# Optimization experiments

Measured on AMD Instinct MI355X. Metric: run time of the kernel, lower is better.

The kernel has to match this reference:

```python
import jax, jax.numpy as jnp
import numpy as np
from jax.scipy.linalg import expm

T, N, M_IN, DT = 8192, 1024, 512, 0.01


def setup_inputs() -> dict:
    key = jax.random.key(0)
    kA, kB, ky, ku = jax.random.split(key, 4)
    ts = jnp.arange(T, dtype=jnp.float32) * DT
    # Mildly stable dynamics so the trajectory stays bounded over T steps.
    A = 0.1 * jax.random.normal(kA, (N, N), jnp.float32) / np.sqrt(N) - 0.5 * jnp.eye(N, dtype=jnp.float32)
    B = jax.random.normal(kB, (N, M_IN), jnp.float32) / np.sqrt(M_IN)
    y0 = jax.random.normal(ky, (N,), jnp.float32)
    u = jax.random.normal(ku, (T, M_IN), jnp.float32)
    return {"ts": ts, "y0": y0, "u": u, "A": A, "B": B}


def reference(ts, y0, u, A, B):
    # Exact solution of dy/dt = A y + B u(t) with u piecewise-linear on ts
    # (what diffrax Tsit5+PID approximates to rtol=1e-3). Uses Van Loan's
    # augmented matrix exponential: z = [y; u; v] with u' = v, v' = 0.
    n = A.shape[0]
    m = B.shape[1]
    h = ts[1] - ts[0]  # uniform grid
    Z_nm = jnp.zeros((n, m), A.dtype)
    Mblk = jnp.block([
        [A, B, Z_nm],
        [jnp.zeros((m, n + m), A.dtype), jnp.eye(m, dtype=A.dtype)],
        [jnp.zeros((m, n + 2 * m), A.dtype)],
    ])
    E = expm(Mblk * h)
    Eyy = E[:n, :n]            # state transition e^{Ah}
    Eyu = E[:n, n:n + m]       # response to constant input u_k
    Eyv = E[:n, n + m:]        # response to input slope v_k
    v = (u[1:] - u[:-1]) / h                     # [T-1, m] slopes
    c = u[:-1] @ Eyu.T + v @ Eyv.T               # [T-1, n] affine terms

    def step(y, ck):
        y_next = Eyy @ y + ck
        return y_next, y_next

    _, ys = jax.lax.scan(step, y0, c)
    return jnp.concatenate([y0[None, :], ys], axis=0)  # [T, n]
```

## Files before the change

### kernel.cpp

```cpp
#include <hip/hip_runtime.h>

#define GT 8192
#define GN 1024
#define GM 512
#define CCH 1024
#define SCH 8

typedef __attribute__((ext_vector_type(8))) short bf16x8;
typedef __attribute__((ext_vector_type(4))) float f32x4;

__device__ __forceinline__ unsigned short f2bf(float x) {
    unsigned int u = __float_as_uint(x);
    u += 0x7FFF + ((u >> 16) & 1);
    return (unsigned short)(u >> 16);
}
__device__ __forceinline__ float bf2f(unsigned short b) {
    return __uint_as_float(((unsigned int)b) << 16);
}
__device__ __forceinline__ void split2(float x, unsigned short& h0, unsigned short& h1) {
    h0 = f2bf(x);
    h1 = f2bf(x - bf2f(h0));
}
__device__ __forceinline__ void split3(float x, unsigned short& s0,
                                       unsigned short& s1, unsigned short& s2) {
    s0 = f2bf(x); float r = x - bf2f(s0);
    s1 = f2bf(r); r -= bf2f(s1);
    s2 = f2bf(r);
}
__device__ __forceinline__ long swz(long e, int sh) {
    return e ^ (((e >> (sh + 1)) & 3) << 3);
}
__device__ __forceinline__ void gl16(const unsigned short* g, unsigned short* l) {
    __builtin_amdgcn_global_load_lds(
        (const __attribute__((address_space(1))) unsigned int*)g,
        (__attribute__((address_space(3))) unsigned int*)l, 16, 0, 0);
}

template <int BM, int WN, int KS>
__global__ __launch_bounds__(512) void gemm_pp(
    const unsigned short* __restrict__ Ap, long apsz, int alda, int aldsh,
    int ashift, int ashiftN,
    const unsigned short* __restrict__ Bp, long bpsz,
    const float* __restrict__ Cf, long cfb, long cfld,
    const unsigned short* __restrict__ Cp, long cpsz, int cmask,
    int bzero, int bsplit, float beta, float betaB,
    float* __restrict__ Of, long ofb, long ofld,
    unsigned short* __restrict__ Pout, long ppsz, int pstep8, int pmode,
    int segN, int zoff,
    int M, float alpha, float alphaB, int asplit, int add_id,
    const unsigned short* __restrict__ Ap2, long apsz2,
    const unsigned short* __restrict__ Bp2,
    unsigned short* __restrict__ Pout2, long ppsz2, int p2off, int seg2,
    unsigned short* __restrict__ PoutT, int tposeN)
{
    constexpr int NQ = 2 * WN;
    constexpr int MTM = BM / 32;
    constexpr int MTN = BM / (WN * 16);
    constexpr int CPW = KS * BM / 32;
    __shared__ __align__(16) unsigned short At[2][KS][2][BM][32];
    __shared__ __align__(16) unsigned short Bt[2][KS][2][BM][32];

    const int tid = threadIdx.x;
    const int lane = tid & 63;
    const int w = tid >> 6;
    const int ksub = w / NQ;
    const int quad = w % NQ;
    const int wr = (quad / WN) * (BM / 2);
    const int wc = (quad % WN) * (BM / WN);
    const int l16 = lane & 15, koff = lane >> 4;
    const int row0 = blockIdx.x * BM;
    const int col0 = blockIdx.y * BM;
    const int lr4 = lane >> 2;
    const int lg = lane & 3;
    const bool s2 = (Ap2 != nullptr) && (row0 >= seg2);
    const bool lead = (KS == 1) || (ksub == 0);

    f32x4 acc[MTM][MTN] = {};

    auto stage = [&](int bsel, int k0) {
        #pragma unroll
        for (int ci = 0; ci < CPW; ++ci) {
            const int c = w * CPW + ci;
            const int op = c / (KS * BM / 8);
            const int rem = c % (KS * BM / 8);
            const int limb = rem / (KS * BM / 16);
            const int rem2 = rem % (KS * BM / 16);
            const int kk = rem2 / (BM / 16);
            const int rb = (rem2 % (BM / 16)) * 16;
            const int lr = rb + lr4;
            const int q = lg ^ ((lr >> 1) & 3);
            long e; int sh; const unsigned short* base;
            if (op == 0) {
                if (!s2) {
                    int ar = row0 + lr;
                    if (ar < ashiftN) { ar -= ashift; if (ar < 0) ar = 0; }
                    e = (long)ar * alda + k0 + kk * 32 + (q << 3); sh = aldsh;
                    base = Ap + (limb ? apsz : 0);
                } else {
                    e = (long)(row0 - seg2 + lr) * 1024 + k0 + kk * 32 + (q << 3); sh = 10;
                    base = Ap2 + (limb ? apsz2 : 0);
                }
            } else {
                e = (long)(col0 + lr) * 1024 + k0 + kk * 32 + (q << 3); sh = 10;
                base = (s2 ? Bp2 : Bp) + (limb ? bpsz : 0);
            }
            long f = swz(e, sh);
            unsigned short* l = (op == 0 ? &At[bsel][kk][limb][rb][0]
                                         : &Bt[bsel][kk][limb][rb][0]);
            gl16(base + f, l);
        }
    };

    stage(0, 0);
    __syncthreads();
    int cur = 0;
    for (int k0 = 0; k0 < 1024; k0 += KS * 32) {
        if (k0 + KS * 32 < 1024) stage(cur ^ 1, k0 + KS * 32);

        const int kk = ksub;
        bf16x8 a0[MTM], a1[MTM], b0[MTN], b1[MTN];
        #pragma unroll
        for (int mi = 0; mi < MTM; ++mi) {
            int lr = wr + mi * 16 + l16;
            int off = (koff ^ ((lr >> 1) & 3)) << 3;
            a0[mi] = *(const bf16x8*)&At[cur][kk][0][lr][off];
            a1[mi] = *(const bf16x8*)&At[cur][kk][1][lr][off];
        }
        #pragma unroll
        for (int ni = 0; ni < MTN; ++ni) {
            int lr = wc + ni * 16 + l16;
            int off = (koff ^ ((lr >> 1) & 3)) << 3;
            b0[ni] = *(const bf16x8*)&Bt[cur][kk][0][lr][off];
            b1[ni] = *(const bf16x8*)&Bt[cur][kk][1][lr][off];
        }
        #pragma unroll
        for (int mi = 0; mi < MTM; ++mi)
            #pragma unroll
            for (int ni = 0; ni < MTN; ++ni) {
                f32x4 cc = acc[mi][ni];
                cc = __builtin_amdgcn_mfma_f32_16x16x32_bf16(a0[mi], b0[ni], cc, 0, 0, 0);
                cc = __builtin_amdgcn_mfma_f32_16x16x32_bf16(a0[mi], b1[ni], cc, 0, 0, 0);
                cc = __builtin_amdgcn_mfma_f32_16x16x32_bf16(a1[mi], b0[ni], cc, 0, 0, 0);
                acc[mi][ni] = cc;
            }
        __syncthreads();
        cur ^= 1;
    }

    if (KS == 2) {
        float* red = (float*)&At[0][0][0][0][0];
        if (ksub == 1) {
            #pragma unroll
            for (int mi = 0; mi < MTM; ++mi)
                #pragma unroll
                for (int ni = 0; ni < MTN; ++ni)
                    *(f32x4*)&red[(((quad * MTM + mi) * MTN + ni) * 64 + lane) * 4] =
                        acc[mi][ni];
        }
        __syncthreads();
        if (ksub == 0) {
            #pragma unroll
            for (int mi = 0; mi < MTM; ++mi)
                #pragma unroll
                for (int ni = 0; ni < MTN; ++ni) {
                    f32x4 o = *(const f32x4*)
                        &red[(((quad * MTM + mi) * MTN + ni) * 64 + lane) * 4];
                    acc[mi][ni][0] += o[0]; acc[mi][ni][1] += o[1];
                    acc[mi][ni][2] += o[2]; acc[mi][ni][3] += o[3];
                }
        }
    }

    const bool tp = (PoutT != nullptr) && (row0 >= tposeN);
    float* T = (float*)&Bt[0][0][0][0][0];

    if (s2) {
        if (lead) {
            #pragma unroll
            for (int mi = 0; mi < MTM; ++mi)
                #pragma unroll
                for (int r = 0; r < 4; ++r) {
                    const int gr = row0 + wr + mi * 16 + koff * 4 + r;
                    if (gr >= M) continue;
                    const int prow = gr - seg2 + p2off;
                    #pragma unroll
                    for (int ni = 0; ni < MTN; ++ni) {
                        const int gc = col0 + wc + ni * 16 + l16;
                        float pv = acc[mi][ni][r];
                        long f = swz((long)prow * 1024 + gc, 10);
                        unsigned short h0 = f2bf(pv);
                        Pout2[f] = h0;
                        Pout2[ppsz2 + f] = f2bf(pv - bf2f(h0));
                        if (tp) T[(wr + mi * 16 + koff * 4 + r) * 65 + gc - col0] = pv;
                    }
                }
        }
    } else {
        if (lead) {
            #pragma unroll
            for (int mi = 0; mi < MTM; ++mi) {
                #pragma unroll
                for (int r = 0; r < 4; ++r) {
                    const int gr = row0 + wr + mi * 16 + koff * 4 + r;
                    if (gr >= M) continue;
                    const int trow = (gr < segN) ? gr + zoff : gr;
                    if (gr < segN && trow >= segN) continue;
                    const float aa = (trow < asplit) ? alpha : alphaB;
                    const float bb = (trow < bzero) ? 0.f
                                    : ((trow < bsplit) ? beta : betaB);
                    #pragma unroll
                    for (int ni = 0; ni < MTN; ++ni) {
                        const int gc = col0 + wc + ni * 16 + l16;
                        float vp = aa * acc[mi][ni][r];
                        float v = vp;
                        if (bb != 0.f) {
                            int crow = trow & cmask;
                            if (Cf) v += bb * Cf[cfb + (long)crow * cfld + gc];
                            else if (Cp) {
                                long f = swz((long)crow * 1024 + gc, 10);
                                v += bb * (bf2f(Cp[f]) + bf2f(Cp[cpsz + f]));
                            }
                        }
                        if (add_id && gr == gc) v += 1.f;
                        if (Of) Of[ofb + (long)trow * ofld + gc] = v;
                        if (Pout && (!pstep8 || (trow & 7) == 0)) {
                            int prow = pstep8 ? (trow >> 3) : trow;
                            long f = swz((long)prow * 1024 + gc, 10);
                            float pv = (pmode == 2) ? vp : v;
                            unsigned short h0 = f2bf(pv);
                            Pout[f] = h0;
                            Pout[ppsz + f] = f2bf(pv - bf2f(h0));
                        }
                        if (tp) T[(wr + mi * 16 + koff * 4 + r) * 65 + gc - col0] = v;
                    }
                }
            }
        }
    }

    if (BM == 64 && tp) {
        __syncthreads();
        if (tid < 256) {
            const int i = tid >> 2;
            const int jb = (tid & 3) * 16;
            const int prow = col0 + i;
            #pragma unroll
            for (int e2 = 0; e2 < 16; ++e2) {
                int j = jb + e2;
                float v = T[j * 65 + i];
                long f = swz((long)prow * 1024 + (row0 - tposeN + j), 10);
                unsigned short h0 = f2bf(v);
                PoutT[f] = h0;
                PoutT[(long)(1 << 20) + f] = f2bf(v - bf2f(h0));
            }
        }
    }
}

__global__ void split_pl_k(const float* __restrict__ X, unsigned short* __restrict__ P,
                           long psz, int ldsh, float s, long cnt)
{
    long i = (long)blockIdx.x * 256 + threadIdx.x;
    if (i >= cnt) return;
    float v = s * X[i];
    long f = swz(i, ldsh);
    unsigned short h0 = f2bf(v);
    P[f] = h0;
    P[psz + f] = f2bf(v - bf2f(h0));
}

__global__ void trsp_k(const float* __restrict__ in, int R, float s, int add_id,
                       unsigned short* __restrict__ P, long psz, int roff)
{
    __shared__ float t[32][33];
    const int tx = threadIdx.x & 31, ty4 = threadIdx.x >> 5;
    const int r0 = blockIdx.x * 32, c0 = blockIdx.y * 32;
    #pragma unroll
    for (int i = 0; i < 4; ++i)
        t[ty4 * 4 + i][tx] = in[(long)(c0 + ty4 * 4 + i) * R + r0 + tx];
    __syncthreads();
    #pragma unroll
    for (int i = 0; i < 4; ++i) {
        int r = r0 + ty4 * 4 + i, c = c0 + tx;
        float v = s * t[tx][ty4 * 4 + i];
        if (add_id && r == c) v += 1.f;
        long f = swz((long)(r + roff) * 1024 + c, 10);
        unsigned short h0 = f2bf(v);
        P[f] = h0;
        P[psz + f] = f2bf(v - bf2f(h0));
    }
}

__global__ void tspp_k(const unsigned short* __restrict__ IN, long ipsz, long irow0,
                       unsigned short* __restrict__ OUT, long opsz)
{
    __shared__ float t[32][33];
    const int tx = threadIdx.x & 31, ty4 = threadIdx.x >> 5;
    const int r0 = blockIdx.x * 32, c0 = blockIdx.y * 32;
    #pragma unroll
    for (int i = 0; i < 4; ++i) {
        long f = swz((irow0 + r0 + ty4 * 4 + i) * 1024 + c0 + tx, 10);
        t[ty4 * 4 + i][tx] = bf2f(IN[f]) + bf2f(IN[ipsz + f]);
    }
    __syncthreads();
    #pragma unroll
    for (int i = 0; i < 4; ++i) {
        int orow = c0 + ty4 * 4 + i;
        long f = swz((long)orow * 1024 + r0 + tx, 10);
        float v = t[tx][ty4 * 4 + i];
        unsigned short h0 = f2bf(v);
        OUT[f] = h0;
        OUT[opsz + f] = f2bf(v - bf2f(h0));
    }
}

__global__ void gtspp_k(const unsigned short* __restrict__ PV, long vpsz,
                        unsigned short* __restrict__ PG, long gpsz, float h)
{
    __shared__ float t[32][33];
    const int tx = threadIdx.x & 31, ty4 = threadIdx.x >> 5;
    const int k0 = blockIdx.x * 32, n0 = blockIdx.y * 32, z = blockIdx.z;
    #pragma unroll
    for (int i = 0; i < 4; ++i) {
        int k = k0 + ty4 * 4 + i, n = n0 + tx;
        long f2 = swz((long)(512 + k) * 1024 + n, 10);
        float v2 = bf2f(PV[f2]) + bf2f(PV[vpsz + f2]);
        float v;
        if (z == 0) {
            long f1 = swz((long)k * 1024 + n, 10);
            v = h * (bf2f(PV[f1]) + bf2f(PV[vpsz + f1]) - v2);
        } else v = h * v2;
        t[ty4 * 4 + i][tx] = v;
    }
    __syncthreads();
    #pragma unroll
    for (int i = 0; i < 4; ++i) {
        int n = n0 + ty4 * 4 + i, kk = z * 512 + k0 + tx;
        long f = swz((long)n * 1024 + kk, 10);
        float v = t[tx][ty4 * 4 + i];
        unsigned short h0 = f2bf(v);
        PG[f] = h0;
        PG[gpsz + f] = f2bf(v - bf2f(h0));
    }
}

__global__ void copy_rows_k(float* __restrict__ dst, long db, long ds,
                            const float* __restrict__ src, long sb, long ss, int ncols)
{
    int r = blockIdx.y;
    int c = blockIdx.x * 256 + threadIdx.x;
    if (c < ncols) dst[db + (long)r * ds + c] = src[sb + (long)r * ss + c];
}

__global__ void add_rows_k(float* __restrict__ dst, long db, long ds,
                           const float* __restrict__ src, int ncols)
{
    int r = blockIdx.y;
    int c = blockIdx.x * 256 + threadIdx.x;
    if (c < ncols) dst[db + (long)r * ds + c] += src[(long)r * ncols + c];
}

__global__ void scale_add_id_k(float* __restrict__ dst, const float* __restrict__ src,
                               float s, int n)
{
    int r = blockIdx.y;
    int c = blockIdx.x * 256 + threadIdx.x;
    if (c < n) dst[(long)r * n + c] = s * src[(long)r * n + c] + ((r == c) ? 1.f : 0.f);
}

__global__ void scale_copy_k(float* __restrict__ dst, const float* __restrict__ src,
                             float s, long cnt)
{
    long i = (long)blockIdx.x * 256 + threadIdx.x;
    if (i < cnt) dst[i] = s * src[i];
}

__global__ void g1g2_k(float* __restrict__ g1, float* __restrict__ g2,
                       const float* __restrict__ v1, const float* __restrict__ v2,
                       float h, long cnt)
{
    long i = (long)blockIdx.x * 256 + threadIdx.x;
    if (i < cnt) {
        float a = v1[i], b = v2[i];
        g1[i] = h * (a - b);
        g2[i] = h * b;
    }
}

template <int BM, int BN, bool TRANSB>
__global__ __launch_bounds__(256) void gemm_mfma(
    const float* __restrict__ A, long ab, long lda,
    const float* __restrict__ B,
    const float* __restrict__ Cin, long cb, long ldc, float beta,
    float* __restrict__ Out, long ob, long ldo,
    int M, int Nn, int K, float alpha, int add_id)
{
    constexpr int LDT = 40;
    __shared__ unsigned short At[3][BM][LDT];
    __shared__ unsigned short Bt[3][BN][LDT];
    const int tid = threadIdx.x;
    const int lane = tid & 63;
    const int wid = tid >> 6;
    const int row0 = blockIdx.x * BM;
    const int col0 = blockIdx.y * BN;
    constexpr int MR = BM / 32;
    constexpr int NR = BN / 32;
    const int wrow = (wid >> 1) * (BM / 2);
    const int wcol = (wid & 1) * (BN / 2);
    const int l16 = lane & 15;
    const int koff = lane >> 4;
    f32x4 acc[MR][NR] = {};

    for (int k0 = 0; k0 < K; k0 += 32) {
        #pragma unroll
        for (int i = 0; i < BM / 32; ++i) {
            int r = i * 32 + (tid >> 3);
            int kl = (tid & 7) * 4;
            int gr = row0 + r;
            float4 v = make_float4(0.f, 0.f, 0.f, 0.f);
            if (gr < M) v = *(const float4*)&A[ab + (long)gr * lda + (k0 + kl)];
            unsigned short h0[4], h1[4], h2[4];
            split3(v.x, h0[0], h1[0], h2[0]);
            split3(v.y, h0[1], h1[1], h2[1]);
            split3(v.z, h0[2], h1[2], h2[2]);
            split3(v.w, h0[3], h1[3], h2[3]);
            *(ushort4*)&At[0][r][kl] = make_ushort4(h0[0], h0[1], h0[2], h0[3]);
            *(ushort4*)&At[1][r][kl] = make_ushort4(h1[0], h1[1], h1[2], h1[3]);
            *(ushort4*)&At[2][r][kl] = make_ushort4(h2[0], h2[1], h2[2], h2[3]);
        }
        if (TRANSB) {
            #pragma unroll
            for (int i = 0; i < BN / 32; ++i) {
                int r = i * 32 + (tid >> 3);
                int kl = (tid & 7) * 4;
                float4 v = *(const float4*)&B[(long)(col0 + r) * K + (k0 + kl)];
                unsigned short h0[4], h1[4], h2[4];
                split3(v.x, h0[0], h1[0], h2[0]);
                split3(v.y, h0[1], h1[1], h2[1]);
                split3(v.z, h0[2], h1[2], h2[2]);
                split3(v.w, h0[3], h1[3], h2[3]);
                *(ushort4*)&Bt[0][r][kl] = make_ushort4(h0[0], h0[1], h0[2], h0[3]);
                *(ushort4*)&Bt[1][r][kl] = make_ushort4(h1[0], h1[1], h1[2], h1[3]);
                *(ushort4*)&Bt[2][r][kl] = make_ushort4(h2[0], h2[1], h2[2], h2[3]);
            }
        } else {
            constexpr int TPK = BN / 4;
            #pragma unroll
            for (int i = 0; i < BN / 32; ++i) {
                int kl = i * (256 / TPK) + tid / TPK;
                int nl = (tid % TPK) * 4;
                float4 v = *(const float4*)&B[(long)(k0 + kl) * Nn + (col0 + nl)];
                unsigned short s0, s1, s2;
                split3(v.x, s0, s1, s2);
                Bt[0][nl + 0][kl] = s0; Bt[1][nl + 0][kl] = s1; Bt[2][nl + 0][kl] = s2;
                split3(v.y, s0, s1, s2);
                Bt[0][nl + 1][kl] = s0; Bt[1][nl + 1][kl] = s1; Bt[2][nl + 1][kl] = s2;
                split3(v.z, s0, s1, s2);
                Bt[0][nl + 2][kl] = s0; Bt[1][nl + 2][kl] = s1; Bt[2][nl + 2][kl] = s2;
                split3(v.w, s0, s1, s2);
                Bt[0][nl + 3][kl] = s0; Bt[1][nl + 3][kl] = s1; Bt[2][nl + 3][kl] = s2;
            }
        }
        __syncthreads();
        bf16x8 bf[NR][3];
        #pragma unroll
        for (int nr = 0; nr < NR; ++nr) {
            int brow = wcol + nr * 16 + l16;
            #pragma unroll
            for (int s = 0; s < 3; ++s)
                bf[nr][s] = *(const bf16x8*)&Bt[s][brow][koff * 8];
        }
        #pragma unroll
        for (int mr = 0; mr < MR; ++mr) {
            int arow = wrow + mr * 16 + l16;
            bf16x8 a0 = *(const bf16x8*)&At[0][arow][koff * 8];
            bf16x8 a1 = *(const bf16x8*)&At[1][arow][koff * 8];
            bf16x8 a2 = *(const bf16x8*)&At[2][arow][koff * 8];
            #pragma unroll
            for (int nr = 0; nr < NR; ++nr) {
                f32x4 c = acc[mr][nr];
                c = __builtin_amdgcn_mfma_f32_16x16x32_bf16(a0, bf[nr][0], c, 0, 0, 0);
                c = __builtin_amdgcn_mfma_f32_16x16x32_bf16(a0, bf[nr][1], c, 0, 0, 0);
                c = __builtin_amdgcn_mfma_f32_16x16x32_bf16(a1, bf[nr][0], c, 0, 0, 0);
                c = __builtin_amdgcn_mfma_f32_16x16x32_bf16(a0, bf[nr][2], c, 0, 0, 0);
                c = __builtin_amdgcn_mfma_f32_16x16x32_bf16(a1, bf[nr][1], c, 0, 0, 0);
                c = __builtin_amdgcn_mfma_f32_16x16x32_bf16(a2, bf[nr][0], c, 0, 0, 0);
                acc[mr][nr] = c;
            }
        }
        __syncthreads();
    }
    #pragma unroll
    for (int mr = 0; mr < MR; ++mr) {
        #pragma unroll
        for (int r = 0; r < 4; ++r) {
            int gr = row0 + wrow + mr * 16 + koff * 4 + r;
            if (gr >= M) continue;
            #pragma unroll
            for (int nr = 0; nr < NR; ++nr) {
                int gc = col0 + wcol + nr * 16 + l16;
                float v = alpha * acc[mr][nr][r];
                if (Cin) v += beta * Cin[cb + (long)gr * ldc + gc];
                if (add_id && gr == gc) v += 1.f;
                Out[ob + (long)gr * ldo + gc] = v;
            }
        }
    }
}

static void fallback_launch(void* const* d_in, void* d_out, void* d_ws,
                            hipStream_t stream)
{
    const float* y0 = (const float*)d_in[1];
    const float* u  = (const float*)d_in[2];
    const float* Am = (const float*)d_in[3];
    const float* Bm = (const float*)d_in[4];
    float* Yout = (float*)d_out;
    float* w = (float*)d_ws;
    const float h = 0.01f;
    const int N = GN;

    float* Eyy = w;
    float* T1  = Eyy + (long)N * N;
    float* T2  = T1  + (long)N * N;
    float* V1  = T2  + (long)N * N;
    float* Vt  = V1  + (long)N * GM;
    float* V2  = Vt  + (long)N * GM;
    float* G1  = V2  + (long)N * GM;
    float* G2  = G1  + (long)N * GM;
    float* Z   = G2  + (long)N * GM;
    float* Zt  = Z   + (long)CCH * N;
    dim3 blk(256);

    auto gemm = [&](bool transb, const float* A, long ab, long lda,
                    const float* B, const float* Cin, long cb, long ldc, float beta,
                    float* Out, long ob, long ldo,
                    int M, int Nn, int K, float alpha, int add_id) {
        if (M > 1536 && (Nn % 128) == 0) {
            dim3 grid((M + 127) / 128, Nn / 128);
            if (transb)
                gemm_mfma<128, 128, true><<<grid, blk, 0, stream>>>(A, ab, lda, B, Cin, cb, ldc, beta, Out, ob, ldo, M, Nn, K, alpha, add_id);
            else
                gemm_mfma<128, 128, false><<<grid, blk, 0, stream>>>(A, ab, lda, B, Cin, cb, ldc, beta, Out, ob, ldo, M, Nn, K, alpha, add_id);
        } else {
            dim3 grid((M + 63) / 64, Nn / 64);
            if (transb)
                gemm_mfma<64, 64, true><<<grid, blk, 0, stream>>>(A, ab, lda, B, Cin, cb, ldc, beta, Out, ob, ldo, M, Nn, K, alpha, add_id);
            else
                gemm_mfma<64, 64, false><<<grid, blk, 0, stream>>>(A, ab, lda, B, Cin, cb, ldc, beta, Out, ob, ldo, M, Nn, K, alpha, add_id);
        }
    };

    scale_add_id_k<<<dim3(4, N), blk, 0, stream>>>(T1, Am, h / 5.f, N);
    {
        float* pc = T1; float* pn = T2;
        for (int k = 4; k >= 1; --k) {
            float* out = (k == 1) ? Eyy : pn;
            gemm(false, Am, 0, N, pc, nullptr, 0, 0, 0.f, out, 0, N, N, N, N, h / (float)k, 1);
            pn = pc; pc = out;
        }
    }
    const long NM = (long)N * GM;
    scale_copy_k<<<dim3((unsigned)((NM + 255) / 256)), blk, 0, stream>>>(V1, Bm, 1.f / 120.f, NM);
    {
        const float f1[4] = {1.f / 24.f, 1.f / 6.f, 0.5f, 1.f};
        float* pc = V1; float* pn = Vt;
        for (int j = 3; j >= 0; --j) {
            gemm(false, Am, 0, N, pc, Bm, 0, GM, f1[3 - j], pn, 0, GM, N, GM, N, h, 0);
            float* t = pc; pc = pn; pn = t;
        }
    }
    scale_copy_k<<<dim3((unsigned)((NM + 255) / 256)), blk, 0, stream>>>(V2, Bm, 1.f / 720.f, NM);
    {
        const float f2[4] = {1.f / 120.f, 1.f / 24.f, 1.f / 6.f, 0.5f};
        float* pc = V2; float* pn = Vt;
        for (int j = 3; j >= 0; --j) {
            gemm(false, Am, 0, N, pc, Bm, 0, GM, f2[3 - j], pn, 0, GM, N, GM, N, h, 0);
            float* t = pc; pc = pn; pn = t;
        }
    }
    g1g2_k<<<dim3((unsigned)((NM + 255) / 256)), blk, 0, stream>>>(G1, G2, V1, V2, h, NM);
    gemm(true, u, 0, GM, G1, nullptr, 0, 0, 0.f, Yout, (long)N, N, GT - 1, N, GM, 1.f, 0);
    gemm(true, u, GM, GM, G2, Yout, (long)N, N, 1.f, Yout, (long)N, N, GT - 1, N, GM, 1.f, 0);
    copy_rows_k<<<dim3(4, 1), blk, 0, stream>>>(Yout, 0, 0, y0, 0, 0, N);
    for (int s = 2; s <= SCH; ++s) {
        int Mr = (GT - 1 - s) / SCH + 1;
        gemm(true, Yout, (long)(s - 1) * N, (long)SCH * N, Eyy,
             Yout, (long)s * N, (long)SCH * N, 1.f,
             Yout, (long)s * N, (long)SCH * N, Mr, N, N, 1.f, 0);
    }
    copy_rows_k<<<dim3(4, 1), blk, 0, stream>>>(Z, 0, 0, y0, 0, 0, N);
    copy_rows_k<<<dim3(4, CCH - 1), blk, 0, stream>>>(Z, (long)N, (long)N,
                                                      Yout, (long)SCH * N, (long)SCH * N, N);
    gemm(false, Eyy, 0, N, Eyy, nullptr, 0, 0, 0.f, T1, 0, N, N, N, N, 1.f, 0);
    gemm(false, T1, 0, N, T1, nullptr, 0, 0, 0.f, T2, 0, N, N, N, N, 1.f, 0);
    gemm(false, T2, 0, N, T2, nullptr, 0, 0, 0.f, T1, 0, N, N, N, N, 1.f, 0);
    {
        float* Mc = T1; float* Mo = T2;
        float* Zc = Z;  float* Zn = Zt;
        for (int p = 0; p < 10; ++p) {
            int o = 1 << p;
            gemm(true, Zc, 0, N, Mc, Zc, (long)o * N, N, 1.f,
                 Zn, (long)o * N, N, CCH - o, N, N, 1.f, 0);
            copy_rows_k<<<dim3(4, o), blk, 0, stream>>>(Zn, 0, N, Zc, 0, N, N);
            if (p < 9) {
                gemm(false, Mc, 0, N, Mc, nullptr, 0, 0, 0.f, Mo, 0, N, N, N, N, 1.f, 0);
                float* t = Mc; Mc = Mo; Mo = t;
            }
            float* t = Zc; Zc = Zn; Zn = t;
        }
        copy_rows_k<<<dim3(4, CCH), blk, 0, stream>>>(Yout, 0, (long)SCH * N, Zc, 0, N, N);
        float* Q = Zc; float* Qt = Zn;
        for (int s = 1; s <= SCH - 1; ++s) {
            gemm(true, Q, 0, N, Eyy, nullptr, 0, 0, 0.f, Qt, 0, N, CCH, N, N, 1.f, 0);
            int Mr = (GT - 1 - s) / SCH + 1;
            add_rows_k<<<dim3(4, Mr), blk, 0, stream>>>(Yout, (long)s * N, (long)SCH * N, Qt, N);
            float* t = Q; Q = Qt; Qt = t;
        }
    }
}

extern "C" void kernel_launch(void* const* d_in, const int* in_sizes, int n_in,
                              void* d_out, int out_size, void* d_ws, size_t ws_size,
                              hipStream_t stream)
{
    (void)in_sizes; (void)n_in; (void)out_size;
    const size_t NEED = 46ull * 1024 * 1024;
    if (ws_size < NEED) { fallback_launch(d_in, d_out, d_ws, stream); return; }

    const float* y0 = (const float*)d_in[1];
    const float* u  = (const float*)d_in[2];
    const float* Am = (const float*)d_in[3];
    const float* Bm = (const float*)d_in[4];
    float* Yout = (float*)d_out;
    char* w = (char*)d_ws;
    const float h = 0.01f;
    const size_t MB = 1024 * 1024;
    const long P1M = 1 << 20;
    const long P2M = 1 << 21;
    const long PUS = 1 << 22;
    const long PBS = 1 << 19;
    const int  BIG = 1 << 30;

    unsigned short* PU   = (unsigned short*)(w);
    unsigned short* PZW1 = (unsigned short*)(w);
    unsigned short* PZW2 = (unsigned short*)(w + 8 * MB);
    unsigned short* CH1  = (unsigned short*)(w + 16 * MB);
    unsigned short* SQb  = (unsigned short*)(w + 16 * MB);
    unsigned short* PWb  = (unsigned short*)(w + 20 * MB);
    unsigned short* CH2  = (unsigned short*)(w + 24 * MB);
    unsigned short* PY1  = (unsigned short*)(w + 24 * MB);
    unsigned short* PY2  = (unsigned short*)(w + 28 * MB);
    unsigned short* PE   = (unsigned short*)(w + 32 * MB);
    unsigned short* PG   = (unsigned short*)(w + 36 * MB);
    unsigned short* SQa  = PG;
    unsigned short* PA   = (unsigned short*)(w + 40 * MB);
    unsigned short* PWa  = PA;
    unsigned short* PBT  = (unsigned short*)(w + 44 * MB);

    dim3 blk(256), blk5(512);

    auto G64 = [&](const unsigned short* Ap, long apsz, int alda, int aldsh,
                   int ashift, int ashiftN,
                   const unsigned short* Bp,
                   const float* Cf, long cfb, long cfld,
                   const unsigned short* Cp, long cpsz, int cmask,
                   int bzero, int bsplit, float beta, float betaB,
                   float* Of, long ofb, long ofld,
                   unsigned short* Pout, long ppsz, int pstep8, int pmode,
                   int segN, int zoff, int M, float alpha, float alphaB,
                   int asplit, int add_id,
                   const unsigned short* Ap2, long apsz2, const unsigned short* Bp2,
                   unsigned short* Pout2, long ppsz2, int p2off, int seg2,
                   unsigned short* PoutT, int tposeN) {
        dim3 grid((M + 63) / 64, 16);
        gemm_pp<64, 2, 2><<<grid, blk5, 0, stream>>>(
            Ap, apsz, alda, aldsh, ashift, ashiftN, Bp, P1M,
            Cf, cfb, cfld, Cp, cpsz, cmask, bzero, bsplit, beta, betaB,
            Of, ofb, ofld, Pout, ppsz, pstep8, pmode, segN, zoff,
            M, alpha, alphaB, asplit, add_id,
            Ap2, apsz2, Bp2, Pout2, ppsz2, p2off, seg2, PoutT, tposeN);
    };

    split_pl_k<<<dim3(4096), blk, 0, stream>>>(Am, PA, P1M, 10, 1.f, (long)1 << 20);

    trsp_k<<<dim3(32, 32), blk, 0, stream>>>(Am, 1024, h / 5.f, 1, CH1, P2M, 0);
    trsp_k<<<dim3(16, 32), blk, 0, stream>>>(Bm, 512, 1.f / 120.f, 0, CH1, P2M, 1024);
    trsp_k<<<dim3(16, 32), blk, 0, stream>>>(Bm, 512, 1.f / 720.f, 0, CH1, P2M, 1536);
    trsp_k<<<dim3(16, 32), blk, 0, stream>>>(Bm, 512, 1.f, 0, PBT, PBS, 0);

    {
        const float alE[4] = {h / 4.f, h / 3.f, h / 2.f, h};
        const float f1[4] = {1.f / 24.f, 1.f / 6.f, 0.5f, 1.f};
        const float f2[4] = {1.f / 120.f, 1.f / 24.f, 1.f / 6.f, 0.5f};
        unsigned short* cc = CH1; unsigned short* cn = CH2;
        for (int j = 0; j < 4; ++j) {
            G64(cc, P2M, 1024, 10, 0, 0, PA,
                nullptr, 0, 0, PBT, PBS, 511,
                1024, 1536, f1[j], f2[j],
                nullptr, 0, 0, cn, P2M, 0, 1,
                BIG, 0, 2048, alE[j], h, 1024, 1,
                nullptr, 0, nullptr, nullptr, 0, 0, BIG, nullptr, BIG);
            unsigned short* t = cc; cc = cn; cn = t;
        }
    }
    tspp_k<<<dim3(32, 32), blk, 0, stream>>>(CH1, P2M, 0, PE, P1M);
    gtspp_k<<<dim3(16, 32, 2), blk, 0, stream>>>(CH1 + (1 << 20), P2M, PG, P1M, h);

    split_pl_k<<<dim3(16384), blk, 0, stream>>>(u, PU, PUS, 9, 1.f, PUS);

    gemm_pp<128, 4, 1><<<dim3(64, 8), blk5, 0, stream>>>(
        PU, PUS, 512, 9, 0, 0, PG, P1M,
        nullptr, 0, 0, nullptr, 0, -1, 0, BIG, 0.f, 0.f,
        Yout, 1024, 1024, PY1, P1M, 1, 1,
        BIG, 0, GT - 1, 1.f, 1.f, BIG, 0,
        nullptr, 0, nullptr, nullptr, 0, 0, BIG, nullptr, BIG);
    copy_rows_k<<<dim3(4, 1), blk, 0, stream>>>(Yout, 0, 0, y0, 0, 0, 1024);

    G64(PY1, P1M, 1024, 10, 0, 0, PE,
        Yout, 2 * 1024, 8192, nullptr, 0, -1, 0, BIG, 1.f, 0.f,
        Yout, 2 * 1024, 8192, PY2, P1M, 0, 1,
        BIG, 0, 2048, 1.f, 1.f, BIG, 0,
        CH1, P2M, PE, SQa, P1M, 0, 1024, PWa, 1024);
    G64(PY2, P1M, 1024, 10, 0, 0, PE,
        Yout, 3 * 1024, 8192, nullptr, 0, -1, 0, BIG, 1.f, 0.f,
        Yout, 3 * 1024, 8192, PY1, P1M, 0, 1,
        BIG, 0, 2048, 1.f, 1.f, BIG, 0,
        SQa, P1M, PWa, SQb, P1M, 0, 1024, PWb, 1024);
    G64(PY1, P1M, 1024, 10, 0, 0, PE,
        Yout, 4 * 1024, 8192, nullptr, 0, -1, 0, BIG, 1.f, 0.f,
        Yout, 4 * 1024, 8192, PY2, P1M, 0, 1,
        BIG, 0, 2048, 1.f, 1.f, BIG, 0,
        SQb, P1M, PWb, PZW1, P2M, 1024, 1024, PWa, 1024);
    {
        unsigned short* pc = PY2; unsigned short* pn = PY1;
        for (int s = 5; s <= 7; ++s) {
            G64(pc, P1M, 1024, 10, 0, 0, PE,
                Yout, (long)s * 1024, 8192, nullptr, 0, -1, 0, BIG, 1.f, 0.f,
                Yout, (long)s * 1024, 8192, pn, P1M, 0, 1,
                BIG, 0, 1024, 1.f, 1.f, BIG, 0,
                nullptr, 0, nullptr, nullptr, 0, 0, BIG, nullptr, BIG);
            unsigned short* t = pc; pc = pn; pn = t;
        }
        G64(pc, P1M, 1024, 10, 0, 0, PE,
            Yout, 0, 8192, nullptr, 0, -1, 0, BIG, 1.f, 0.f,
            Yout, 0, 8192, PZW1, P2M, 0, 1,
            BIG, 1, 1023, 1.f, 1.f, BIG, 0,
            nullptr, 0, nullptr, nullptr, 0, 0, BIG, nullptr, BIG);
    }
    split_pl_k<<<dim3(4), blk, 0, stream>>>(y0, PZW1, P2M, 10, 1.f, 1024);

    {
        unsigned short* PZc = PZW1; unsigned short* PZn = PZW2;
        for (int p = 0; p < 10; ++p) {
            int o = 1 << p;
            unsigned short* PWcur = (p & 1) ? PWb : PWa;
            unsigned short* PWnxt = (p & 1) ? PWa : PWb;
            if (p < 9) {
                G64(PZc, P2M, 1024, 10, o, 1024, PWcur,
                    nullptr, 0, 0, PZc, P2M, 0x7fffffff,
                    0, 1024, 1.f, 0.f,
                    nullptr, 0, 0, PZn, P2M, 0, 1,
                    1024, 0, 2048, 0.f, 1.f, o, 0,
                    nullptr, 0, nullptr, nullptr, 0, 0, BIG, PWnxt, 1024);
            } else {
                G64(PZc, P2M, 1024, 10, o, 1024, PWcur,
                    nullptr, 0, 0, PZc, P2M, 0x7fffffff,
                    0, 1024, 1.f, 0.f,
                    Yout, 0, 8192, PZn, P2M, 0, 1,
                    1024, 0, 1024, 0.f, 1.f, o, 0,
                    nullptr, 0, nullptr, nullptr, 0, 0, BIG, nullptr, BIG);
            }
            unsigned short* t = PZc; PZc = PZn; PZn = t;
        }
    }
    copy_rows_k<<<dim3(4, 1), blk, 0, stream>>>(Yout, 0, 0, y0, 0, 0, 1024);

    {
        const unsigned short* pc = PZW1; long apsz = P2M;
        unsigned short* pn = PY1;
        for (int s = 1; s <= 7; ++s) {
            G64(pc, apsz, 1024, 10, 0, 0, PE,
                Yout, (long)s * 1024, 8192, nullptr, 0, -1, 0, BIG, 1.f, 0.f,
                Yout, (long)s * 1024, 8192,
                (s < 7) ? pn : nullptr, P1M, 0, 2,
                BIG, 0, 1024, 1.f, 1.f, BIG, 0,
                nullptr, 0, nullptr, nullptr, 0, 0, BIG, nullptr, BIG);
            pc = pn; apsz = P1M;
            pn = (pn == PY1) ? PY2 : PY1;
        }
    }
}
```

Before: 808.5 us.

## Batch final propagation steps using precomputed powers of the transition matrix

Adds segment-indexed B-matrix strides, row masks and output strides to the GEMM kernel, so one launch can apply different matrices to different 1024-row segments. The prologue now also computes extra powers of Eyy (PW2, PW3, PW4, via PWR=PE). The final seven serial propagation GEMMs become two wider batched launches: one multiplies by E^1..E^4 in parallel, the other applies E^4 to those results. This trades a serial launch chain for more parallel work per launch, with extra power-matrix computation, more workspace aliasing and some risk to accuracy.

```diff
diff --git a/kernel.cpp b/kernel.cpp
--- a/kernel.cpp
+++ b/kernel.cpp
@@ -39,14 +39,14 @@
 template <int BM, int WN, int KS>
 __global__ __launch_bounds__(512) void gemm_pp(
     const unsigned short* __restrict__ Ap, long apsz, int alda, int aldsh,
-    int ashift, int ashiftN,
-    const unsigned short* __restrict__ Bp, long bpsz,
+    int amask, int ashift, int ashiftN,
+    const unsigned short* __restrict__ Bp, long bpsz, long bstride,
     const float* __restrict__ Cf, long cfb, long cfld,
     const unsigned short* __restrict__ Cp, long cpsz, int cmask,
     int bzero, int bsplit, float beta, float betaB,
-    float* __restrict__ Of, long ofb, long ofld,
-    unsigned short* __restrict__ Pout, long ppsz, int pstep8, int pmode,
-    int segN, int zoff,
+    float* __restrict__ Of, long ofb, long ofld, long ofstep,
+    unsigned short* __restrict__ Pout, long ppsz, int pstep8, int pmode, int prowstep,
+    int segN, int zoff, int trmask,
     int M, float alpha, float alphaB, int asplit, int add_id,
     const unsigned short* __restrict__ Ap2, long apsz2,
     const unsigned short* __restrict__ Bp2,
@@ -74,6 +74,7 @@
     const int lg = lane & 3;
     const bool s2 = (Ap2 != nullptr) && (row0 >= seg2);
     const bool lead = (KS == 1) || (ksub == 0);
+    const int segk = row0 >> 10;
 
     f32x4 acc[MTM][MTN] = {};
 
@@ -92,7 +93,7 @@
             long e; int sh; const unsigned short* base;
             if (op == 0) {
                 if (!s2) {
-                    int ar = row0 + lr;
+                    int ar = (row0 + lr) & amask;
                     if (ar < ashiftN) { ar -= ashift; if (ar < 0) ar = 0; }
                     e = (long)ar * alda + k0 + kk * 32 + (q << 3); sh = aldsh;
                     base = Ap + (limb ? apsz : 0);
@@ -102,7 +103,7 @@
                 }
             } else {
                 e = (long)(col0 + lr) * 1024 + k0 + kk * 32 + (q << 3); sh = 10;
-                base = (s2 ? Bp2 : Bp) + (limb ? bpsz : 0);
+                base = (s2 ? Bp2 : (Bp + (long)segk * bstride)) + (limb ? bpsz : 0);
             }
             long f = swz(e, sh);
             unsigned short* l = (op == 0 ? &At[bsel][kk][limb][rb][0]
@@ -187,23 +188,27 @@
                     for (int ni = 0; ni < MTN; ++ni) {
                         const int gc = col0 + wc + ni * 16 + l16;
                         float pv = acc[mi][ni][r];
-                        long f = swz((long)prow * 1024 + gc, 10);
-                        unsigned short h0 = f2bf(pv);
-                        Pout2[f] = h0;
-                        Pout2[ppsz2 + f] = f2bf(pv - bf2f(h0));
+                        if (Pout2) {
+                            long f = swz((long)prow * 1024 + gc, 10);
+                            unsigned short h0 = f2bf(pv);
+                            Pout2[f] = h0;
+                            Pout2[ppsz2 + f] = f2bf(pv - bf2f(h0));
+                        }
                         if (tp) T[(wr + mi * 16 + koff * 4 + r) * 65 + gc - col0] = pv;
                     }
                 }
         }
     } else {
         if (lead) {
+            const long ofe = ofb + (long)segk * ofstep;
+            const long cfe = cfb + (long)segk * ofstep;
             #pragma unroll
             for (int mi = 0; mi < MTM; ++mi) {
                 #pragma unroll
                 for (int r = 0; r < 4; ++r) {
                     const int gr = row0 + wr + mi * 16 + koff * 4 + r;
                     if (gr >= M) continue;
-                    const int trow = (gr < segN) ? gr + zoff : gr;
+                    const int trow = (((gr < segN) ? gr + zoff : gr)) & trmask;
                     if (gr < segN && trow >= segN) continue;
                     const float aa = (trow < asplit) ? alpha : alphaB;
                     const float bb = (trow < bzero) ? 0.f
@@ -215,16 +220,16 @@
                         float v = vp;
                         if (bb != 0.f) {
                             int crow = trow & cmask;
-                            if (Cf) v += bb * Cf[cfb + (long)crow * cfld + gc];
+                            if (Cf) v += bb * Cf[cfe + (long)crow * cfld + gc];
                             else if (Cp) {
                                 long f = swz((long)crow * 1024 + gc, 10);
                                 v += bb * (bf2f(Cp[f]) + bf2f(Cp[cpsz + f]));
                             }
                         }
                         if (add_id && gr == gc) v += 1.f;
-                        if (Of) Of[ofb + (long)trow * ofld + gc] = v;
+                        if (Of) Of[ofe + (long)trow * ofld + gc] = v;
                         if (Pout && (!pstep8 || (trow & 7) == 0)) {
-                            int prow = pstep8 ? (trow >> 3) : trow;
+                            int prow = (pstep8 ? (trow >> 3) : trow) + segk * prowstep;
                             long f = swz((long)prow * 1024 + gc, 10);
                             float pv = (pmode == 2) ? vp : v;
                             unsigned short h0 = f2bf(pv);
@@ -636,57 +641,40 @@
     char* w = (char*)d_ws;
     const float h = 0.01f;
     const size_t MB = 1024 * 1024;
-    const long P1M = 1 << 20;
-    const long P2M = 1 << 21;
+    const long PP  = 1 << 20;
+    const long P2  = 1 << 21;
+    const long P4  = 1 << 22;
     const long PUS = 1 << 22;
     const long PBS = 1 << 19;
     const int  BIG = 1 << 30;
 
     unsigned short* PU   = (unsigned short*)(w);
     unsigned short* PZW1 = (unsigned short*)(w);
+    unsigned short* PA   = (unsigned short*)(w + 8 * MB);
+    unsigned short* SQa  = (unsigned short*)(w + 8 * MB);
+    unsigned short* SQb  = (unsigned short*)(w + 12 * MB);
     unsigned short* PZW2 = (unsigned short*)(w + 8 * MB);
     unsigned short* CH1  = (unsigned short*)(w + 16 * MB);
-    unsigned short* SQb  = (unsigned short*)(w + 16 * MB);
-    unsigned short* PWb  = (unsigned short*)(w + 20 * MB);
+    unsigned short* WA   = (unsigned short*)(w + 16 * MB);
+    unsigned short* PWt0 = (unsigned short*)(w + 20 * MB);
     unsigned short* CH2  = (unsigned short*)(w + 24 * MB);
-    unsigned short* PY1  = (unsigned short*)(w + 24 * MB);
-    unsigned short* PY2  = (unsigned short*)(w + 28 * MB);
-    unsigned short* PE   = (unsigned short*)(w + 32 * MB);
-    unsigned short* PG   = (unsigned short*)(w + 36 * MB);
-    unsigned short* SQa  = PG;
-    unsigned short* PA   = (unsigned short*)(w + 40 * MB);
-    unsigned short* PWa  = PA;
+    unsigned short* WB   = (unsigned short*)(w + 24 * MB);
+    unsigned short* PE   = (unsigned short*)(w + 28 * MB);
+    unsigned short* PG   = (unsigned short*)(w + 32 * MB);
+    unsigned short* PW2  = PG;
+    unsigned short* PW3  = (unsigned short*)(w + 36 * MB);
+    unsigned short* PW4  = (unsigned short*)(w + 40 * MB);
     unsigned short* PBT  = (unsigned short*)(w + 44 * MB);
+    unsigned short* QPL  = (unsigned short*)(w + 8 * MB);
+    unsigned short* PWR  = PE;
 
     dim3 blk(256), blk5(512);
 
-    auto G64 = [&](const unsigned short* Ap, long apsz, int alda, int aldsh,
-                   int ashift, int ashiftN,
-                   const unsigned short* Bp,
-                   const float* Cf, long cfb, long cfld,
-                   const unsigned short* Cp, long cpsz, int cmask,
-                   int bzero, int bsplit, float beta, float betaB,
-                   float* Of, long ofb, long ofld,
-                   unsigned short* Pout, long ppsz, int pstep8, int pmode,
-                   int segN, int zoff, int M, float alpha, float alphaB,
-                   int asplit, int add_id,
-                   const unsigned short* Ap2, long apsz2, const unsigned short* Bp2,
-                   unsigned short* Pout2, long ppsz2, int p2off, int seg2,
-                   unsigned short* PoutT, int tposeN) {
-        dim3 grid((M + 63) / 64, 16);
-        gemm_pp<64, 2, 2><<<grid, blk5, 0, stream>>>(
-            Ap, apsz, alda, aldsh, ashift, ashiftN, Bp, P1M,
-            Cf, cfb, cfld, Cp, cpsz, cmask, bzero, bsplit, beta, betaB,
-            Of, ofb, ofld, Pout, ppsz, pstep8, pmode, segN, zoff,
-            M, alpha, alphaB, asplit, add_id,
-            Ap2, apsz2, Bp2, Pout2, ppsz2, p2off, seg2, PoutT, tposeN);
-    };
-
-    split_pl_k<<<dim3(4096), blk, 0, stream>>>(Am, PA, P1M, 10, 1.f, (long)1 << 20);
-
-    trsp_k<<<dim3(32, 32), blk, 0, stream>>>(Am, 1024, h / 5.f, 1, CH1, P2M, 0);
-    trsp_k<<<dim3(16, 32), blk, 0, stream>>>(Bm, 512, 1.f / 120.f, 0, CH1, P2M, 1024);
-    trsp_k<<<dim3(16, 32), blk, 0, stream>>>(Bm, 512, 1.f / 720.f, 0, CH1, P2M, 1536);
+    split_pl_k<<<dim3(4096), blk, 0, stream>>>(Am, PA, PP, 10, 1.f, (long)1 << 20);
+
+    trsp_k<<<dim3(32, 32), blk, 0, stream>>>(Am, 1024, h / 5.f, 1, CH1, P2, 0);
+    trsp_k<<<dim3(16, 32), blk, 0, stream>>>(Bm, 512, 1.f / 120.f, 0, CH1, P2, 1024);
+    trsp_k<<<dim3(16, 32), blk, 0, stream>>>(Bm, 512, 1.f / 720.f, 0, CH1, P2, 1536);
     trsp_k<<<dim3(16, 32), blk, 0, stream>>>(Bm, 512, 1.f, 0, PBT, PBS, 0);
 
     {
@@ -695,99 +683,149 @@
         const float f2[4] = {1.f / 120.f, 1.f / 24.f, 1.f / 6.f, 0.5f};
         unsigned short* cc = CH1; unsigned short* cn = CH2;
         for (int j = 0; j < 4; ++j) {
-            G64(cc, P2M, 1024, 10, 0, 0, PA,
+            gemm_pp<64, 2, 2><<<dim3(32, 16), blk5, 0, stream>>>(
+                cc, P2, 1024, 10, -1, 0, 0,
+                PA, PP, 0,
                 nullptr, 0, 0, PBT, PBS, 511,
                 1024, 1536, f1[j], f2[j],
-                nullptr, 0, 0, cn, P2M, 0, 1,
-                BIG, 0, 2048, alE[j], h, 1024, 1,
+                nullptr, 0, 0, 0,
+                cn, P2, 0, 1, 0,
+                BIG, 0, -1,
+                2048, alE[j], h, 1024, 1,
                 nullptr, 0, nullptr, nullptr, 0, 0, BIG, nullptr, BIG);
             unsigned short* t = cc; cc = cn; cn = t;
         }
     }
-    tspp_k<<<dim3(32, 32), blk, 0, stream>>>(CH1, P2M, 0, PE, P1M);
-    gtspp_k<<<dim3(16, 32, 2), blk, 0, stream>>>(CH1 + (1 << 20), P2M, PG, P1M, h);
+    tspp_k<<<dim3(32, 32), blk, 0, stream>>>(CH1, P2, 0, PE, PP);
+    gtspp_k<<<dim3(16, 32, 2), blk, 0, stream>>>(CH1 + (1 << 20), P2, PG, PP, h);
 
     split_pl_k<<<dim3(16384), blk, 0, stream>>>(u, PU, PUS, 9, 1.f, PUS);
 
     gemm_pp<128, 4, 1><<<dim3(64, 8), blk5, 0, stream>>>(
-        PU, PUS, 512, 9, 0, 0, PG, P1M,
-        nullptr, 0, 0, nullptr, 0, -1, 0, BIG, 0.f, 0.f,
-        Yout, 1024, 1024, PY1, P1M, 1, 1,
-        BIG, 0, GT - 1, 1.f, 1.f, BIG, 0,
+        PU, PUS, 512, 9, -1, 0, 0,
+        PG, PP, 0,
+        nullptr, 0, 0, nullptr, 0, -1,
+        0, BIG, 0.f, 0.f,
+        Yout, 1024, 1024, 0,
+        WB, PP, 1, 1, 0,
+        BIG, 0, -1,
+        GT - 1, 1.f, 1.f, BIG, 0,
         nullptr, 0, nullptr, nullptr, 0, 0, BIG, nullptr, BIG);
-    copy_rows_k<<<dim3(4, 1), blk, 0, stream>>>(Yout, 0, 0, y0, 0, 0, 1024);
-
-    G64(PY1, P1M, 1024, 10, 0, 0, PE,
-        Yout, 2 * 1024, 8192, nullptr, 0, -1, 0, BIG, 1.f, 0.f,
-        Yout, 2 * 1024, 8192, PY2, P1M, 0, 1,
-        BIG, 0, 2048, 1.f, 1.f, BIG, 0,
-        CH1, P2M, PE, SQa, P1M, 0, 1024, PWa, 1024);
-    G64(PY2, P1M, 1024, 10, 0, 0, PE,
-        Yout, 3 * 1024, 8192, nullptr, 0, -1, 0, BIG, 1.f, 0.f,
-        Yout, 3 * 1024, 8192, PY1, P1M, 0, 1,
-        BIG, 0, 2048, 1.f, 1.f, BIG, 0,
-        SQa, P1M, PWa, SQb, P1M, 0, 1024, PWb, 1024);
-    G64(PY1, P1M, 1024, 10, 0, 0, PE,
-        Yout, 4 * 1024, 8192, nullptr, 0, -1, 0, BIG, 1.f, 0.f,
-        Yout, 4 * 1024, 8192, PY2, P1M, 0, 1,
-        BIG, 0, 2048, 1.f, 1.f, BIG, 0,
-        SQb, P1M, PWb, PZW1, P2M, 1024, 1024, PWa, 1024);
-    {
-        unsigned short* pc = PY2; unsigned short* pn = PY1;
-        for (int s = 5; s <= 7; ++s) {
-            G64(pc, P1M, 1024, 10, 0, 0, PE,
-                Yout, (long)s * 1024, 8192, nullptr, 0, -1, 0, BIG, 1.f, 0.f,
-                Yout, (long)s * 1024, 8192, pn, P1M, 0, 1,
-                BIG, 0, 1024, 1.f, 1.f, BIG, 0,
-                nullptr, 0, nullptr, nullptr, 0, 0, BIG, nullptr, BIG);
-            unsigned short* t = pc; pc = pn; pn = t;
-        }
-        G64(pc, P1M, 1024, 10, 0, 0, PE,
-            Yout, 0, 8192, nullptr, 0, -1, 0, BIG, 1.f, 0.f,
-            Yout, 0, 8192, PZW1, P2M, 0, 1,
-            BIG, 1, 1023, 1.f, 1.f, BIG, 0,
-            nullptr, 0, nullptr, nullptr, 0, 0, BIG, nullptr, BIG);
-    }
-    split_pl_k<<<dim3(4), blk, 0, stream>>>(y0, PZW1, P2M, 10, 1.f, 1024);
+
+    gemm_pp<64, 2, 2><<<dim3(32, 16), blk5, 0, stream>>>(
+        WB, PP, 1024, 10, -1, 0, 0,
+        PE, PP, 0,
+        Yout, 2 * 1024, 8192, nullptr, 0, -1,
+        0, BIG, 1.f, 0.f,
+        Yout, 2 * 1024, 8192, 0,
+        PW3, PP, 0, 1, 0,
+        BIG, 0, -1,
+        2048, 1.f, 1.f, BIG, 0,
+        CH1, P2, PE, SQa, PP, 0, 1024, PW2, 1024);
+    gemm_pp<64, 2, 2><<<dim3(32, 16), blk5, 0, stream>>>(
+        PW3, PP, 1024, 10, -1, 0, 0,
+        PE, PP, 0,
+        Yout, 3 * 1024, 8192, nullptr, 0, -1,
+        0, BIG, 1.f, 0.f,
+        Yout, 3 * 1024, 8192, 0,
+        WB, PP, 0, 1, 0,
+        BIG, 0, -1,
+        2048, 1.f, 1.f, BIG, 0,
+        SQa, PP, PW2, SQb, PP, 0, 1024, PW4, 1024);
+    gemm_pp<64, 2, 2><<<dim3(32, 16), blk5, 0, stream>>>(
+        WB, PP, 1024, 10, -1, 0, 0,
+        PE, PP, 0,
+        Yout, 4 * 1024, 8192, nullptr, 0, -1,
+        0, BIG, 1.f, 0.f,
+        Yout, 4 * 1024, 8192, 0,
+        WA, PP, 0, 1, 0,
+        BIG, 0, -1,
+        2048, 1.f, 1.f, BIG, 0,
+        SQb, PP, PW4, PZW1, P2, 1024, 1024, PWt0, 1024);
+    gemm_pp<64, 2, 2><<<dim3(32, 16), blk5, 0, stream>>>(
+        WA, PP, 1024, 10, -1, 0, 0,
+        PE, PP, 0,
+        Yout, 5 * 1024, 8192, nullptr, 0, -1,
+        0, BIG, 1.f, 0.f,
+        Yout, 5 * 1024, 8192, 0,
+        WB, PP, 0, 1, 0,
+        BIG, 0, -1,
+        2048, 1.f, 1.f, BIG, 0,
+        SQa, PP, PE, nullptr, 0, 0, 1024, PW3, 1024);
+    gemm_pp<64, 2, 2><<<dim3(16, 16), blk5, 0, stream>>>(
+        WB, PP, 1024, 10, -1, 0, 0,
+        PE, PP, 0,
+        Yout, 6 * 1024, 8192, nullptr, 0, -1,
+        0, BIG, 1.f, 0.f,
+        Yout, 6 * 1024, 8192, 0,
+        WA, PP, 0, 1, 0,
+        BIG, 0, -1,
+        1024, 1.f, 1.f, BIG, 0,
+        nullptr, 0, nullptr, nullptr, 0, 0, BIG, nullptr, BIG);
+    gemm_pp<64, 2, 2><<<dim3(16, 16), blk5, 0, stream>>>(
+        WA, PP, 1024, 10, -1, 0, 0,
+        PE, PP, 0,
+        Yout, 7 * 1024, 8192, nullptr, 0, -1,
+        0, BIG, 1.f, 0.f,
+        Yout, 7 * 1024, 8192, 0,
+        WB, PP, 0, 1, 0,
+        BIG, 0, -1,
+        1024, 1.f, 1.f, BIG, 0,
+        nullptr, 0, nullptr, nullptr, 0, 0, BIG, nullptr, BIG);
+    gemm_pp<64, 2, 2><<<dim3(16, 16), blk5, 0, stream>>>(
+        WB, PP, 1024, 10, -1, 0, 0,
+        PE, PP, 0,
+        Yout, 0, 8192, nullptr, 0, -1,
+        0, BIG, 1.f, 0.f,
+        Yout, 0, 8192, 0,
+        PZW1, P2, 0, 1, 0,
+        BIG, 1, -1,
+        1023, 1.f, 1.f, BIG, 0,
+        nullptr, 0, nullptr, nullptr, 0, 0, BIG, nullptr, BIG);
+    split_pl_k<<<dim3(4), blk, 0, stream>>>(y0, PZW1, P2, 10, 1.f, 1024);
 
     {
         unsigned short* PZc = PZW1; unsigned short* PZn = PZW2;
         for (int p = 0; p < 10; ++p) {
             int o = 1 << p;
-            unsigned short* PWcur = (p & 1) ? PWb : PWa;
-            unsigned short* PWnxt = (p & 1) ? PWa : PWb;
-            if (p < 9) {
-                G64(PZc, P2M, 1024, 10, o, 1024, PWcur,
-                    nullptr, 0, 0, PZc, P2M, 0x7fffffff,
-                    0, 1024, 1.f, 0.f,
-                    nullptr, 0, 0, PZn, P2M, 0, 1,
-                    1024, 0, 2048, 0.f, 1.f, o, 0,
-                    nullptr, 0, nullptr, nullptr, 0, 0, BIG, PWnxt, 1024);
-            } else {
-                G64(PZc, P2M, 1024, 10, o, 1024, PWcur,
-                    nullptr, 0, 0, PZc, P2M, 0x7fffffff,
-                    0, 1024, 1.f, 0.f,
-                    Yout, 0, 8192, PZn, P2M, 0, 1,
-                    1024, 0, 1024, 0.f, 1.f, o, 0,
-                    nullptr, 0, nullptr, nullptr, 0, 0, BIG, nullptr, BIG);
-            }
+            int Mr = (p == 9) ? 1024 : 2048;
+            unsigned short* PWc = (p & 1) ? WA : PWt0;
+            unsigned short* PWn = (p & 1) ? PWt0 : WA;
+            gemm_pp<64, 2, 2><<<dim3(Mr / 64, 16), blk5, 0, stream>>>(
+                PZc, P2, 1024, 10, -1, o, 1024,
+                PWc, PP, 0,
+                nullptr, 0, 0,
+                PZc, P2, 0x7fffffff,
+                0, 1024, 1.f, 0.f,
+                (p == 9) ? Yout : nullptr, 0, 8192, 0,
+                PZn, P2, 0, 1, 0,
+                1024, 0, -1,
+                Mr, 0.f, 1.f, o, 0,
+                nullptr, 0, nullptr, nullptr, 0, 0, BIG,
+                (p < 9) ? PWn : nullptr, 1024);
             unsigned short* t = PZc; PZc = PZn; PZn = t;
         }
     }
     copy_rows_k<<<dim3(4, 1), blk, 0, stream>>>(Yout, 0, 0, y0, 0, 0, 1024);
 
-    {
-        const unsigned short* pc = PZW1; long apsz = P2M;
-        unsigned short* pn = PY1;
-        for (int s = 1; s <= 7; ++s) {
-            G64(pc, apsz, 1024, 10, 0, 0, PE,
-                Yout, (long)s * 1024, 8192, nullptr, 0, -1, 0, BIG, 1.f, 0.f,
-                Yout, (long)s * 1024, 8192,
-                (s < 7) ? pn : nullptr, P1M, 0, 2,
-                BIG, 0, 1024, 1.f, 1.f, BIG, 0,
-                nullptr, 0, nullptr, nullptr, 0, 0, BIG, nullptr, BIG);
-            pc = pn; apsz = P1M;
-            pn = (pn == PY1) ? PY2 : PY1;
-        }
-    }
-}
+    gemm_pp<64, 2, 2><<<dim3(64, 16), blk5, 0, stream>>>(
+        PZW1, P2, 1024, 10, 1023, 0, 0,
+        PWR, PP, (long)(1 << 21),
+        Yout, 1024, 8192, nullptr, 0, -1,
+        0, BIG, 1.f, 0.f,
+        Yout, 1024, 8192, 1024,
+        QPL, P4, 0, 2, 1024,
+        0, 0, 1023,
+        4096, 1.f, 1.f, BIG, 0,
+        nullptr, 0, nullptr, nullptr, 0, 0, BIG, nullptr, BIG);
+    gemm_pp<64, 2, 2><<<dim3(48, 16), blk5, 0, stream>>>(
+        QPL, P4, 1024, 10, -1, 0, 0,
+        PW4, PP, 0,
+        Yout, 5 * 1024, 8192, nullptr, 0, -1,
+        0, BIG, 1.f, 0.f,
+        Yout, 5 * 1024, 8192, 1024,
+        nullptr, 0, 0, 1, 0,
+        0, 0, 1023,
+        3072, 1.f, 1.f, BIG, 0,
+        nullptr, 0, nullptr, nullptr, 0, 0, BIG, nullptr, BIG);
+}
```

After: 758.0 us. 6.2% less time.
